# Performance work log

Hardware: AMD Instinct MI355X
Metric: run time of the kernel (lower is better)

The kernel has to match this reference:

```python
import jax, jax.numpy as jnp
import numpy as np


def _laplacian(A):
    # D^{-1/2} A D^{-1/2}; original builds diag matrices and does D@A@D,
    # which is mathematically identical to broadcast row/col scaling.
    d = jnp.sum(A, axis=-1)
    dinv = 1.0 / jnp.sqrt(d)
    return A * dinv[:, None] * dinv[None, :]


def _poly(A, theta):
    # P = I + sum_{i=1..k} theta_sig[i-1] * A^i  (theta passed through sigmoid)
    t = jax.nn.sigmoid(theta)
    N = A.shape[-1]
    P = jnp.eye(N, dtype=A.dtype)
    seg = P
    for i in range(theta.shape[0]):  # k is small (2), static loop over poly order
        seg = seg @ A
        P = P + seg * t[i]
    return P


def setup_inputs() -> dict:
    key = jax.random.key(0)
    k1, k2, k3, k4 = jax.random.split(key, 4)
    N, DIN, DOUT, K_CHEB = 4096, 64, 64, 2
    return {
        "x": jax.random.normal(k1, (N, DIN), dtype=jnp.float32),
        "A": jax.random.uniform(k2, (N, N), dtype=jnp.float32),  # positive row sums
        "theta": jax.random.normal(k3, (K_CHEB,), dtype=jnp.float32),
        "W": jax.random.normal(k4, (DOUT, DIN), dtype=jnp.float32) / np.float32(np.sqrt(DIN)),
        "b": jnp.zeros((DOUT,), dtype=jnp.float32),
        "k": 4,
    }


def reference(x, A, theta, W, b, k):
    S = _laplacian(A)
    S = _poly(S, theta)
    S = _laplacian(S)
    # double argsort over last dim = per-row descending rank of each entry
    rank = jnp.argsort(jnp.argsort(-S, axis=-1), axis=-1)
    mask = jnp.where(rank < k, jnp.float32(1.0), jnp.float32(0.0))
    S = S * mask  # keep only top-k entries per row
    x = S @ x     # [N,N] @ [N,DIN]
    return x @ W.T + b  # nn.Linear
```

## Files before the change

### kernel.cpp

```cpp
#include <hip/hip_runtime.h>
#include <hip/hip_bf16.h>
#include <float.h>
#include <math.h>

#define N 4096
#define DIN 64

typedef signed char i8_t;
typedef signed char i8x4 __attribute__((ext_vector_type(4)));
typedef int i32x4 __attribute__((ext_vector_type(4)));
typedef float f32x4 __attribute__((ext_vector_type(4)));

__device__ __forceinline__ void gload16(const void* g, void* l) {
    __builtin_amdgcn_global_load_lds((const __attribute__((address_space(1))) void*)g,
                                     (__attribute__((address_space(3))) void*)l,
                                     16, 0, 0);
}

__device__ __forceinline__ float block_reduce_sum(float s) {
    __shared__ float red[4];
    #pragma unroll
    for (int off = 32; off; off >>= 1) s += __shfl_down(s, off);
    if ((threadIdx.x & 63) == 0) red[threadIdx.x >> 6] = s;
    __syncthreads();
    return red[0] + red[1] + red[2] + red[3];
}

__device__ __forceinline__ bool better(float v1, int j1, float v2, int j2) {
    return v1 > v2 || (v1 == v2 && j1 < j2);
}
__device__ __forceinline__ void ins4(float v, int j, float bv[4], int bj[4]) {
    if (!better(v, j, bv[3], bj[3])) return;
    bv[3] = v; bj[3] = j;
    if (better(bv[3], bj[3], bv[2], bj[2])) {
        float tv = bv[2]; int tj = bj[2]; bv[2] = bv[3]; bj[2] = bj[3]; bv[3] = tv; bj[3] = tj;
    }
    if (better(bv[2], bj[2], bv[1], bj[1])) {
        float tv = bv[1]; int tj = bj[1]; bv[1] = bv[2]; bj[1] = bj[2]; bv[2] = tv; bj[2] = tj;
    }
    if (better(bv[1], bj[1], bv[0], bj[0])) {
        float tv = bv[0]; int tj = bj[0]; bv[0] = bv[1]; bj[0] = bj[1]; bv[1] = tv; bj[1] = tj;
    }
}

__global__ __launch_bounds__(256) void k_rowsum_dinv(const float* __restrict__ A,
                                                     float* __restrict__ dinv,
                                                     float* __restrict__ rowsumP) {
    int row = blockIdx.x, tid = threadIdx.x;
    const float4* a4 = (const float4*)(A + (size_t)row * N);
    float s = 0.f;
    for (int j = tid; j < N / 4; j += 256) {
        float4 v = a4[j];
        s += v.x + v.y + v.z + v.w;
    }
    float tot = block_reduce_sum(s);
    if (tid == 0) {
        dinv[row] = rsqrtf(tot);
        rowsumP[row] = 0.f;
    }
}

__global__ __launch_bounds__(1024) void k_dmax(const float* __restrict__ dinv,
                                               float* __restrict__ dmaxf) {
    int t = threadIdx.x;
    float m = fmaxf(fmaxf(dinv[t], dinv[t + 1024]), fmaxf(dinv[t + 2048], dinv[t + 3072]));
    #pragma unroll
    for (int off = 32; off; off >>= 1) m = fmaxf(m, __shfl_down(m, off));
    __shared__ float red[16];
    if ((t & 63) == 0) red[t >> 6] = m;
    __syncthreads();
    if (t == 0) {
        float mm = red[0];
        #pragma unroll
        for (int i = 1; i < 16; i++) mm = fmaxf(mm, red[i]);
        *dmaxf = mm;
    }
}

__global__ __launch_bounds__(256) void k_make_sqt(const float* __restrict__ A,
                                                  const float* __restrict__ dinv,
                                                  const float* __restrict__ dmaxf,
                                                  i8_t* __restrict__ Sq,
                                                  i8_t* __restrict__ Tq) {
    __shared__ float tile[64][65];
    int tid = threadIdx.x;
    int c4 = tid & 15;
    int rg = tid >> 4;
    int i0 = blockIdx.y * 64;
    int j0 = blockIdx.x * 64;
    float dmax = *dmaxf;
    float sinv = 127.0f / (dmax * dmax);
    float4 dj = *(const float4*)(dinv + j0 + 4 * c4);
    #pragma unroll
    for (int rr = 0; rr < 4; rr++) {
        int r = rg + 16 * rr;
        int row = i0 + r;
        float di = dinv[row];
        float4 av = *(const float4*)(A + (size_t)row * N + j0 + 4 * c4);
        float s0 = av.x * di * dj.x, s1 = av.y * di * dj.y;
        float s2 = av.z * di * dj.z, s3 = av.w * di * dj.w;
        i8x4 qv;
        qv[0] = (i8_t)(int)fminf(rintf(s0 * sinv), 127.f);
        qv[1] = (i8_t)(int)fminf(rintf(s1 * sinv), 127.f);
        qv[2] = (i8_t)(int)fminf(rintf(s2 * sinv), 127.f);
        qv[3] = (i8_t)(int)fminf(rintf(s3 * sinv), 127.f);
        *(i8x4*)(Sq + (size_t)row * N + j0 + 4 * c4) = qv;
        tile[r][4 * c4 + 0] = s0;
        tile[r][4 * c4 + 1] = s1;
        tile[r][4 * c4 + 2] = s2;
        tile[r][4 * c4 + 3] = s3;
    }
    __syncthreads();
    #pragma unroll
    for (int cc = 0; cc < 4; cc++) {
        int c = rg + 16 * cc;
        int gj = j0 + c;
        i8x4 qv;
        #pragma unroll
        for (int u = 0; u < 4; u++)
            qv[u] = (i8_t)(int)fminf(rintf(tile[4 * c4 + u][c] * sinv), 127.f);
        *(i8x4*)(Tq + (size_t)gj * N + i0 + 4 * c4) = qv;
    }
}

__global__ __launch_bounds__(256) void k_gemm(const i8_t* __restrict__ Sq,
                                              const i8_t* __restrict__ Tq,
                                              const float* __restrict__ dmaxf,
                                              const float* __restrict__ theta,
                                              float* __restrict__ rowsumP,
                                              float* __restrict__ candV,
                                              int* __restrict__ candJ) {
    __shared__ i8_t As[128 * 64];
    __shared__ i8_t Bs[128 * 64];
    __shared__ float pbuf[128][65];
    int tid = threadIdx.x;
    int lane = tid & 63;
    int wave = tid >> 6;
    int wr = wave >> 1, wc = wave & 1;
    int bi = blockIdx.x, bj = blockIdx.y;

    int qoff = ((tid & 3) ^ ((tid >> 3) & 3)) * 16;
    int row0 = tid >> 2;
    const i8_t* Ag0 = Sq + (size_t)(bi * 128 + row0) * N + qoff;
    const i8_t* Ag1 = Sq + (size_t)(bi * 128 + 64 + row0) * N + qoff;
    const i8_t* Bg0 = Tq + (size_t)(bj * 128 + row0) * N + qoff;
    const i8_t* Bg1 = Tq + (size_t)(bj * 128 + 64 + row0) * N + qoff;
    i8_t* Al0 = As + tid * 16;
    i8_t* Al1 = As + (tid + 256) * 16;
    i8_t* Bl0 = Bs + tid * 16;
    i8_t* Bl1 = Bs + (tid + 256) * 16;

    i32x4 acc[4][4];
    i32x4 z = {0, 0, 0, 0};
    #pragma unroll
    for (int i = 0; i < 4; i++)
        #pragma unroll
        for (int j = 0; j < 4; j++) acc[i][j] = z;

    int r = lane & 15, q = lane >> 4;
    int qs = q ^ ((r >> 1) & 3);
    int aoff = (wr * 64 + r) * 64 + qs * 16;
    int boff = (wc * 64 + r) * 64 + qs * 16;

    for (int k0 = 0; k0 < N; k0 += 64) {
        __syncthreads();
        gload16(Ag0 + k0, Al0);
        gload16(Ag1 + k0, Al1);
        gload16(Bg0 + k0, Bl0);
        gload16(Bg1 + k0, Bl1);
        __syncthreads();
        i32x4 af[4], bfr[4];
        #pragma unroll
        for (int mi = 0; mi < 4; mi++) af[mi] = *(const i32x4*)(As + aoff + mi * 16 * 64);
        #pragma unroll
        for (int ni = 0; ni < 4; ni++) bfr[ni] = *(const i32x4*)(Bs + boff + ni * 16 * 64);
        #pragma unroll
        for (int mi = 0; mi < 4; mi++)
            #pragma unroll
            for (int ni = 0; ni < 4; ni++)
                acc[mi][ni] = __builtin_amdgcn_mfma_i32_16x16x64_i8(af[mi], bfr[ni],
                                                                    acc[mi][ni], 0, 0, 0);
    }

    float dmax = *dmaxf;
    float sq = dmax * dmax / 127.0f;
    float t0 = 1.f / (1.f + expf(-theta[0]));
    float t1 = 1.f / (1.f + expf(-theta[1]));
    float t0s = t0 * sq;
    float t1s2 = t1 * sq * sq;
    int col = lane & 15, quad = lane >> 4;

    #pragma unroll
    for (int mi = 0; mi < 4; mi++) {
        int gi0 = bi * 128 + wr * 64 + mi * 16 + quad * 4;
        float rsum[4] = {0.f, 0.f, 0.f, 0.f};
        #pragma unroll
        for (int ni = 0; ni < 4; ni++) {
            int gj = bj * 128 + wc * 64 + ni * 16 + col;
            f32x4 pf;
            #pragma unroll
            for (int rr = 0; rr < 4; rr++) {
                int gi = gi0 + rr;
                float qv = (float)Sq[(size_t)gi * N + gj];
                float p = t1s2 * (float)acc[mi][ni][rr] + t0s * qv + ((gi == gj) ? 1.f : 0.f);
                pf[rr] = p;
                rsum[rr] += p;
            }
            acc[mi][ni] = __builtin_bit_cast(i32x4, pf);
        }
        #pragma unroll
        for (int rr = 0; rr < 4; rr++) {
            float v = rsum[rr];
            v += __shfl_xor(v, 1);
            v += __shfl_xor(v, 2);
            v += __shfl_xor(v, 4);
            v += __shfl_xor(v, 8);
            if (col == 0) atomicAdd(&rowsumP[gi0 + rr], v);
        }
    }

    float bv[4] = {-FLT_MAX, -FLT_MAX, -FLT_MAX, -FLT_MAX};
    int bjx[4] = {N, N, N, N};
    int srow = tid >> 1;
    int shalf = tid & 1;

    #pragma unroll
    for (int pass = 0; pass < 2; pass++) {
        if (wc == pass) {
            #pragma unroll
            for (int mi = 0; mi < 4; mi++) {
                int prow = wr * 64 + mi * 16 + quad * 4;
                #pragma unroll
                for (int ni = 0; ni < 4; ni++) {
                    f32x4 pf = __builtin_bit_cast(f32x4, acc[mi][ni]);
                    #pragma unroll
                    for (int rr = 0; rr < 4; rr++)
                        pbuf[prow + rr][ni * 16 + col] = pf[rr];
                }
            }
        }
        __syncthreads();
        int jbase = bj * 128 + pass * 64 + shalf * 32;
        for (int i = 0; i < 32; i++)
            ins4(pbuf[srow][shalf * 32 + i], jbase + i, bv, bjx);
        __syncthreads();
    }

    float ov[4]; int oj[4];
    #pragma unroll
    for (int c = 0; c < 4; c++) { ov[c] = __shfl_xor(bv[c], 1); oj[c] = __shfl_xor(bjx[c], 1); }
    #pragma unroll
    for (int c = 0; c < 4; c++) ins4(ov[c], oj[c], bv, bjx);
    if (shalf == 0) {
        size_t base = ((size_t)(bi * 128 + srow) * 32 + bj) * 4;
        #pragma unroll
        for (int c = 0; c < 4; c++) { candV[base + c] = bv[c]; candJ[base + c] = bjx[c]; }
    }
}

__global__ __launch_bounds__(256) void k_dinv2(const float* __restrict__ rowsumP,
                                               float* __restrict__ dinv2) {
    int g = blockIdx.x * 256 + threadIdx.x;
    dinv2[g] = rsqrtf(rowsumP[g]);
}

__global__ __launch_bounds__(64) void k_final(const float* __restrict__ candV,
                                              const int* __restrict__ candJ,
                                              const float* __restrict__ dinv2,
                                              const float* __restrict__ x,
                                              const float* __restrict__ W,
                                              const float* __restrict__ bvec,
                                              const int* __restrict__ kin,
                                              float* __restrict__ out) {
    int row = blockIdx.x, t = threadIdx.x;
    float2 cv = *(const float2*)(candV + (size_t)row * 128 + t * 2);
    int2 cj = *(const int2*)(candJ + (size_t)row * 128 + t * 2);
    float bv[4] = {-FLT_MAX, -FLT_MAX, -FLT_MAX, -FLT_MAX};
    int bj[4] = {N, N, N, N};
    ins4(cv.x * dinv2[cj.x], cj.x, bv, bj);
    ins4(cv.y * dinv2[cj.y], cj.y, bv, bj);
    #pragma unroll
    for (int off = 1; off < 64; off <<= 1) {
        float ov[4]; int oj[4];
        #pragma unroll
        for (int c = 0; c < 4; c++) { ov[c] = __shfl_xor(bv[c], off); oj[c] = __shfl_xor(bj[c], off); }
        #pragma unroll
        for (int c = 0; c < 4; c++) ins4(ov[c], oj[c], bv, bj);
    }
    int kk = kin[0];
    if (kk > 4) kk = 4;
    if (kk < 0) kk = 0;
    float sc = dinv2[row];
    float y = 0.f;
    for (int c = 0; c < kk; c++)
        y += sc * bv[c] * x[(size_t)bj[c] * DIN + t];
    __shared__ float ys[DIN];
    ys[t] = y;
    __syncthreads();
    const float4* w4 = (const float4*)(W + (size_t)t * DIN);
    const float4* y4 = (const float4*)ys;
    float o = bvec[t];
    #pragma unroll
    for (int d = 0; d < DIN / 4; d++) {
        float4 wv = w4[d], yv = y4[d];
        o += wv.x * yv.x + wv.y * yv.y + wv.z * yv.z + wv.w * yv.w;
    }
    out[(size_t)row * DIN + t] = o;
}

extern "C" void kernel_launch(void* const* d_in, const int* in_sizes, int n_in,
                              void* d_out, int out_size, void* d_ws, size_t ws_size,
                              hipStream_t stream) {
    const float* x = (const float*)d_in[0];
    const float* A = (const float*)d_in[1];
    const float* theta = (const float*)d_in[2];
    const float* W = (const float*)d_in[3];
    const float* b = (const float*)d_in[4];
    const int* kin = (const int*)d_in[5];
    float* out = (float*)d_out;

    char* ws = (char*)d_ws;
    i8_t* Sq = (i8_t*)ws;
    i8_t* Tq = (i8_t*)(ws + (size_t)N * N);
    float* candV = (float*)(ws + (size_t)N * N * 2);
    int* candJ = (int*)(ws + (size_t)N * N * 2 + (size_t)N * 128 * 4);
    float* dinv = (float*)(ws + (size_t)N * N * 2 + (size_t)N * 128 * 8);
    float* dinv2 = dinv + N;
    float* rowsumP = dinv2 + N;
    float* dmaxf = rowsumP + N;

    k_rowsum_dinv<<<N, 256, 0, stream>>>(A, dinv, rowsumP);
    k_dmax<<<1, 1024, 0, stream>>>(dinv, dmaxf);
    k_make_sqt<<<dim3(64, 64), 256, 0, stream>>>(A, dinv, dmaxf, Sq, Tq);
    k_gemm<<<dim3(32, 32), 256, 0, stream>>>(Sq, Tq, dmaxf, theta, rowsumP, candV, candJ);
    k_dinv2<<<N / 256, 256, 0, stream>>>(rowsumP, dinv2);
    k_final<<<N, 64, 0, stream>>>(candV, candJ, dinv2, x, W, b, kin, out);
}
```

Baseline: 276.9 us.

## Precompute second normalization via column sums, drop atomics and alias GEMM shared memory

The row sums of the polynomial matrix P are computed up front as Sq·colsum(Tq) plus the row sum of Sq, using two new small kernels. This removes the per-tile atomicAdd of row sums from the GEMM. The GEMM now scales candidates by the column factor dinv2 before the per-tile top-k, so k_final no longer gathers dinv2 per candidate. The GEMM also reuses the int8 staging shared memory for the top-k buffer, which lowers LDS use and may raise occupancy. The cost is two extra passes over the int8 matrices.

Result: no change. 279.3 us (+0.8%).

```diff
diff --git a/kernel.cpp b/kernel.cpp
--- a/kernel.cpp
+++ b/kernel.cpp
@@ -24,6 +24,18 @@
     if ((threadIdx.x & 63) == 0) red[threadIdx.x >> 6] = s;
     __syncthreads();
     return red[0] + red[1] + red[2] + red[3];
+}
+
+__device__ __forceinline__ float2 block_reduce_sum2(float a, float b) {
+    __shared__ float reda[4], redb[4];
+    #pragma unroll
+    for (int off = 32; off; off >>= 1) { a += __shfl_down(a, off); b += __shfl_down(b, off); }
+    if ((threadIdx.x & 63) == 0) { reda[threadIdx.x >> 6] = a; redb[threadIdx.x >> 6] = b; }
+    __syncthreads();
+    float2 r;
+    r.x = reda[0] + reda[1] + reda[2] + reda[3];
+    r.y = redb[0] + redb[1] + redb[2] + redb[3];
+    return r;
 }
 
 __device__ __forceinline__ bool better(float v1, int j1, float v2, int j2) {
@@ -44,8 +56,7 @@
 }
 
 __global__ __launch_bounds__(256) void k_rowsum_dinv(const float* __restrict__ A,
-                                                     float* __restrict__ dinv,
-                                                     float* __restrict__ rowsumP) {
+                                                     float* __restrict__ dinv) {
     int row = blockIdx.x, tid = threadIdx.x;
     const float4* a4 = (const float4*)(A + (size_t)row * N);
     float s = 0.f;
@@ -54,10 +65,7 @@
         s += v.x + v.y + v.z + v.w;
     }
     float tot = block_reduce_sum(s);
-    if (tid == 0) {
-        dinv[row] = rsqrtf(tot);
-        rowsumP[row] = 0.f;
-    }
+    if (tid == 0) dinv[row] = rsqrtf(tot);
 }
 
 __global__ __launch_bounds__(1024) void k_dmax(const float* __restrict__ dinv,
@@ -123,16 +131,58 @@
     }
 }
 
+__global__ __launch_bounds__(256) void k_colsum(const i8_t* __restrict__ Tq,
+                                                float* __restrict__ colsumQ) {
+    int row = blockIdx.x, tid = threadIdx.x;
+    int4 w = ((const int4*)(Tq + (size_t)row * N))[tid];
+    int s = 0;
+    #pragma unroll
+    for (int u = 0; u < 4; u++) {
+        int wv = (u == 0) ? w.x : (u == 1) ? w.y : (u == 2) ? w.z : w.w;
+        s += (int)(i8_t)(wv) + (int)(i8_t)(wv >> 8) + (int)(i8_t)(wv >> 16) + (int)(i8_t)(wv >> 24);
+    }
+    float tot = block_reduce_sum((float)s);
+    if (tid == 0) colsumQ[row] = tot;
+}
+
+__global__ __launch_bounds__(256) void k_dinv2row(const i8_t* __restrict__ Sq,
+                                                  const float* __restrict__ colsumQ,
+                                                  const float* __restrict__ dmaxf,
+                                                  const float* __restrict__ theta,
+                                                  float* __restrict__ dinv2) {
+    int row = blockIdx.x, tid = threadIdx.x;
+    int4 w = ((const int4*)(Sq + (size_t)row * N))[tid];
+    float dot = 0.f, rq = 0.f;
+    #pragma unroll
+    for (int u = 0; u < 4; u++) {
+        int wv = (u == 0) ? w.x : (u == 1) ? w.y : (u == 2) ? w.z : w.w;
+        float4 cv = ((const float4*)colsumQ)[tid * 4 + u];
+        float q0 = (float)(i8_t)(wv), q1 = (float)(i8_t)(wv >> 8);
+        float q2 = (float)(i8_t)(wv >> 16), q3 = (float)(i8_t)(wv >> 24);
+        dot += q0 * cv.x + q1 * cv.y + q2 * cv.z + q3 * cv.w;
+        rq += q0 + q1 + q2 + q3;
+    }
+    float2 tot = block_reduce_sum2(dot, rq);
+    if (tid == 0) {
+        float dmax = *dmaxf;
+        float sqv = dmax * dmax / 127.0f;
+        float t0 = 1.f / (1.f + expf(-theta[0]));
+        float t1 = 1.f / (1.f + expf(-theta[1]));
+        dinv2[row] = rsqrtf(t1 * sqv * sqv * tot.x + t0 * sqv * tot.y + 1.f);
+    }
+}
+
 __global__ __launch_bounds__(256) void k_gemm(const i8_t* __restrict__ Sq,
                                               const i8_t* __restrict__ Tq,
                                               const float* __restrict__ dmaxf,
                                               const float* __restrict__ theta,
-                                              float* __restrict__ rowsumP,
+                                              const float* __restrict__ dinv2,
                                               float* __restrict__ candV,
                                               int* __restrict__ candJ) {
-    __shared__ i8_t As[128 * 64];
-    __shared__ i8_t Bs[128 * 64];
-    __shared__ float pbuf[128][65];
+    __shared__ __align__(16) char smem[128 * 65 * 4];
+    i8_t* As = (i8_t*)smem;
+    i8_t* Bs = (i8_t*)(smem + 128 * 64);
+    float (*pbuf)[65] = (float (*)[65])smem;
     int tid = threadIdx.x;
     int lane = tid & 63;
     int wave = tid >> 6;
@@ -181,41 +231,32 @@
                 acc[mi][ni] = __builtin_amdgcn_mfma_i32_16x16x64_i8(af[mi], bfr[ni],
                                                                     acc[mi][ni], 0, 0, 0);
     }
+    __syncthreads();
 
     float dmax = *dmaxf;
-    float sq = dmax * dmax / 127.0f;
+    float sqv = dmax * dmax / 127.0f;
     float t0 = 1.f / (1.f + expf(-theta[0]));
     float t1 = 1.f / (1.f + expf(-theta[1]));
-    float t0s = t0 * sq;
-    float t1s2 = t1 * sq * sq;
+    float t0s = t0 * sqv;
+    float t1s2 = t1 * sqv * sqv;
     int col = lane & 15, quad = lane >> 4;
 
     #pragma unroll
     for (int mi = 0; mi < 4; mi++) {
         int gi0 = bi * 128 + wr * 64 + mi * 16 + quad * 4;
-        float rsum[4] = {0.f, 0.f, 0.f, 0.f};
         #pragma unroll
         for (int ni = 0; ni < 4; ni++) {
             int gj = bj * 128 + wc * 64 + ni * 16 + col;
+            float djv = dinv2[gj];
             f32x4 pf;
             #pragma unroll
             for (int rr = 0; rr < 4; rr++) {
                 int gi = gi0 + rr;
                 float qv = (float)Sq[(size_t)gi * N + gj];
                 float p = t1s2 * (float)acc[mi][ni][rr] + t0s * qv + ((gi == gj) ? 1.f : 0.f);
-                pf[rr] = p;
-                rsum[rr] += p;
+                pf[rr] = p * djv;
             }
             acc[mi][ni] = __builtin_bit_cast(i32x4, pf);
-        }
-        #pragma unroll
-        for (int rr = 0; rr < 4; rr++) {
-            float v = rsum[rr];
-            v += __shfl_xor(v, 1);
-            v += __shfl_xor(v, 2);
-            v += __shfl_xor(v, 4);
-            v += __shfl_xor(v, 8);
-            if (col == 0) atomicAdd(&rowsumP[gi0 + rr], v);
         }
     }
 
@@ -258,12 +299,6 @@
     }
 }
 
-__global__ __launch_bounds__(256) void k_dinv2(const float* __restrict__ rowsumP,
-                                               float* __restrict__ dinv2) {
-    int g = blockIdx.x * 256 + threadIdx.x;
-    dinv2[g] = rsqrtf(rowsumP[g]);
-}
-
 __global__ __launch_bounds__(64) void k_final(const float* __restrict__ candV,
                                               const int* __restrict__ candJ,
                                               const float* __restrict__ dinv2,
@@ -277,8 +312,8 @@
     int2 cj = *(const int2*)(candJ + (size_t)row * 128 + t * 2);
     float bv[4] = {-FLT_MAX, -FLT_MAX, -FLT_MAX, -FLT_MAX};
     int bj[4] = {N, N, N, N};
-    ins4(cv.x * dinv2[cj.x], cj.x, bv, bj);
-    ins4(cv.y * dinv2[cj.y], cj.y, bv, bj);
+    ins4(cv.x, cj.x, bv, bj);
+    ins4(cv.y, cj.y, bv, bj);
     #pragma unroll
     for (int off = 1; off < 64; off <<= 1) {
         float ov[4]; int oj[4];
@@ -326,13 +361,14 @@
     int* candJ = (int*)(ws + (size_t)N * N * 2 + (size_t)N * 128 * 4);
     float* dinv = (float*)(ws + (size_t)N * N * 2 + (size_t)N * 128 * 8);
     float* dinv2 = dinv + N;
-    float* rowsumP = dinv2 + N;
-    float* dmaxf = rowsumP + N;
-
-    k_rowsum_dinv<<<N, 256, 0, stream>>>(A, dinv, rowsumP);
+    float* colsumQ = dinv2 + N;
+    float* dmaxf = colsumQ + N;
+
+    k_rowsum_dinv<<<N, 256, 0, stream>>>(A, dinv);
     k_dmax<<<1, 1024, 0, stream>>>(dinv, dmaxf);
     k_make_sqt<<<dim3(64, 64), 256, 0, stream>>>(A, dinv, dmaxf, Sq, Tq);
-    k_gemm<<<dim3(32, 32), 256, 0, stream>>>(Sq, Tq, dmaxf, theta, rowsumP, candV, candJ);
-    k_dinv2<<<N / 256, 256, 0, stream>>>(rowsumP, dinv2);
+    k_colsum<<<N, 256, 0, stream>>>(Tq, colsumQ);
+    k_dinv2row<<<N, 256, 0, stream>>>(Sq, colsumQ, dmaxf, theta, dinv2);
+    k_gemm<<<dim3(32, 32), 256, 0, stream>>>(Sq, Tq, dmaxf, theta, dinv2, candV, candJ);
     k_final<<<N, 64, 0, stream>>>(candV, candJ, dinv2, x, W, b, kin, out);
 }
```
